# Kernel tuning notes

Measured on AMD Instinct MI355X. Metric: run time of the kernel, lower is better.

## Reference

```python
import jax, jax.numpy as jnp
import numpy as np

B, L, D = 32, 1024, 1024
NEG = -1.0e9


def setup_inputs() -> dict:
    key = jax.random.key(0)
    ks = jax.random.split(key, 12)
    s = 1.0 / np.sqrt(D)
    # random prefix lengths in [L//2, L] -> prefix-ones attention mask
    lengths = jax.random.randint(ks[0], (B,), L // 2, L + 1)
    attention_mask = (jnp.arange(L)[None, :] < lengths[:, None]).astype(jnp.int32)
    return {
        "output": jax.random.normal(ks[1], (B, L, D), jnp.float32),
        "context": jax.random.normal(ks[2], (B, L, D), jnp.float32),
        "attention_mask": attention_mask,
        "Wo": jax.random.uniform(ks[3], (D, D), jnp.float32, -s, s),   # output_trans
        "bo": jnp.zeros((D,), jnp.float32),
        "Wc": jax.random.uniform(ks[4], (D, D), jnp.float32, -s, s),   # context_trans
        "bc": jnp.zeros((D,), jnp.float32),
        "Wb": jax.random.uniform(ks[5], (D, D), jnp.float32, -s, s),   # bilinear (no bias)
        "Wu": jax.random.uniform(ks[6], (1, D), jnp.float32, -s, s),   # U
        "bu": jnp.zeros((1,), jnp.float32),
        "Wv": jax.random.uniform(ks[7], (1, D), jnp.float32, -s, s),   # V
        "bv": jnp.zeros((1,), jnp.float32),
        "Wf": jax.random.uniform(ks[8], (D, 2 * D), jnp.float32, -s, s),  # fc: 2D -> D
        "bf": jnp.zeros((D,), jnp.float32),
    }


def reference(output, context, attention_mask, Wo, bo, Wc, bc, Wb, Wu, bu, Wv, bv, Wf, bf):
    mask_f = attention_mask.astype(output.dtype)          # [B,L]
    lengths = jnp.sum(mask_f, axis=-1)                    # [B]
    key_padding = jnp.where(attention_mask > 0, 0.0, NEG).astype(output.dtype)  # [B,L]

    o_t = output @ Wo.T + bo                              # [B,L,D] output_trans
    c_t = context @ Wc.T + bc                             # [B,L,D] context_trans
    # biaffine: bilinear(o_t) @ c_t^T + U(output) + V(context)^T
    attn = jnp.einsum("bqd,bkd->bqk", o_t @ Wb.T, c_t)    # [B,L,L]
    attn = attn + (output @ Wu.T + bu)                    # [B,L,1] broadcast over keys
    attn = attn + jnp.swapaxes(context @ Wv.T + bv, 1, 2) # [B,1,L] broadcast over queries
    attn = attn + key_padding[:, None, :]
    attn = jax.nn.softmax(attn, axis=-1)

    mix = jnp.einsum("bqk,bkd->bqd", attn, context)       # [B,L,D]
    combined = jnp.concatenate([output, mix], axis=-1)    # [B,L,2D]
    out = jnp.tanh(combined @ Wf.T + bf)                  # [B,L,D]
    # masked mean pooling over sequence
    pooled = jnp.sum(out * mask_f[:, :, None], axis=1) / lengths[:, None]  # [B,D]
    return pooled
```

## Files before the change

### kernel.cpp

```cpp
#include <hip/hip_runtime.h>
#include <hip/hip_fp16.h>
#include <cstdint>
#include <initializer_list>

#define BATCH 32
#define LSEQ 1024
#define DDIM 1024

typedef unsigned short u16;
typedef unsigned int u32;
typedef __bf16 bf16x8 __attribute__((ext_vector_type(8)));
typedef float f32x4 __attribute__((ext_vector_type(4)));

__device__ __forceinline__ u16 f2bf(float f) {
  u32 u = __float_as_uint(f);
  u32 r = (u + 0x7FFFu + ((u >> 16) & 1u)) >> 16;
  return (u16)r;
}
__device__ __forceinline__ float bf2f(u16 h) {
  return __uint_as_float(((u32)h) << 16);
}
__device__ __forceinline__ float tanh_fast(float x) {
  float xx = fminf(fmaxf(x, -15.f), 15.f);
  float t = __expf(2.f * xx);
  return (t - 1.f) / (t + 1.f);
}

__device__ __forceinline__ void gload_lds16(const void* g, void* l) {
  __builtin_amdgcn_global_load_lds(
      (__attribute__((address_space(1))) void*)(uintptr_t)g,
      (__attribute__((address_space(3))) void*)(u32)(uintptr_t)l,
      16, 0, 0);
}

__global__ __launch_bounds__(256) void len_kernel(const int* __restrict__ amask,
                                                  int* __restrict__ lenb) {
  int b = blockIdx.x;
  int4 m = ((const int4*)(amask + (size_t)b * LSEQ))[threadIdx.x];
  int s = m.x + m.y + m.z + m.w;
#pragma unroll
  for (int o = 32; o; o >>= 1) s += __shfl_xor(s, o);
  __shared__ int r[4];
  if ((threadIdx.x & 63) == 0) r[threadIdx.x >> 6] = s;
  __syncthreads();
  if (threadIdx.x == 0) lenb[b] = (r[0] + r[1]) + (r[2] + r[3]);
}

__global__ __launch_bounds__(256) void cvt_kernel(const float* __restrict__ in,
                                                  u16* __restrict__ out, int n4) {
  int i = blockIdx.x * 256 + threadIdx.x;
  if (i >= n4) return;
  float4 f = ((const float4*)in)[i];
  ushort4 o;
  o.x = f2bf(f.x); o.y = f2bf(f.y); o.z = f2bf(f.z); o.w = f2bf(f.w);
  ((ushort4*)out)[i] = o;
}

__global__ __launch_bounds__(256) void transpose_cv(const float* __restrict__ in,
                                                    u16* __restrict__ outT,
                                                    u16* __restrict__ outN,
                                                    const float* __restrict__ wv2,
                                                    float* __restrict__ vpart,
                                                    int vn) {
  __shared__ u16 tile[64][65];
  size_t boff = (size_t)blockIdx.z * (LSEQ * DDIM);
  int k0 = blockIdx.x * 64;
  int d0 = blockIdx.y * 64;
  int tx = threadIdx.x & 63;
  int ty = threadIdx.x >> 6;
  float wv = vpart ? wv2[d0 + tx] : 0.f;
#pragma unroll
  for (int r = ty; r < 64; r += 4) {
    float f = in[boff + (size_t)(k0 + r) * DDIM + d0 + tx];
    u16 h = f2bf(f);
    tile[r][tx] = h;
    if (outN) outN[boff + (size_t)(k0 + r) * DDIM + d0 + tx] = h;
    if (vpart) {
      float p = f * wv;
#pragma unroll
      for (int o = 32; o; o >>= 1) p += __shfl_xor(p, o);
      if (tx == 0) vpart[(size_t)blockIdx.y * vn + blockIdx.z * LSEQ + k0 + r] = p;
    }
  }
  __syncthreads();
#pragma unroll
  for (int r = ty; r < 64; r += 4)
    outT[boff + (size_t)(d0 + r) * LSEQ + k0 + tx] = tile[tx][r];
}

__global__ __launch_bounds__(256) void vred_kernel(const float* __restrict__ vpart,
                                                   float* __restrict__ vbuf, int vn) {
  int i = blockIdx.x * 256 + threadIdx.x;
  if (i >= vn) return;
  float s = 0.f;
#pragma unroll
  for (int p = 0; p < 16; ++p) s += vpart[(size_t)p * vn + i];
  vbuf[i] = s;
}

__global__ __launch_bounds__(256) void rowdot_kernel(const float* __restrict__ x,
                                                     const float* __restrict__ w,
                                                     float* __restrict__ out) {
  int row = blockIdx.x;
  const float* p = x + (size_t)row * DDIM;
  int tid = threadIdx.x;
  float4 a = ((const float4*)p)[tid];
  float4 ww = ((const float4*)w)[tid];
  float s = a.x * ww.x + a.y * ww.y + a.z * ww.z + a.w * ww.w;
#pragma unroll
  for (int o = 32; o; o >>= 1) s += __shfl_xor(s, o);
  __shared__ float r[4];
  if ((tid & 63) == 0) r[tid >> 6] = s;
  __syncthreads();
  if (tid == 0) out[row] = (r[0] + r[1]) + (r[2] + r[3]);
}

__global__ __launch_bounds__(256) void w2_kernel(const float* __restrict__ Wv,
                                                 const float* __restrict__ bbo,
                                                 const float* __restrict__ Wc,
                                                 float* __restrict__ wv2) {
  int d = blockIdx.x * 256 + threadIdx.x;
  float s = Wv[d];
  for (int e = 0; e < DDIM; ++e) s += bbo[e] * Wc[(size_t)e * DDIM + d];
  wv2[d] = s;
}

template <int OUT_F32, int HAS_BIAS, int DO_TANH, int ZBATCH>
__global__ __launch_bounds__(256) void gemm_nt(
    const u16* __restrict__ A1, const u16* __restrict__ A2, int ksplit,
    const u16* __restrict__ Bw, const float* __restrict__ bias,
    void* __restrict__ Cout, int K, int lda, int ldb, int ldc,
    long long sA, long long sB, long long sC, int nm, int nn, int nz) {
  __shared__ u16 As[4096];
  __shared__ u16 Bs[4096];

  const int id = blockIdx.x;
  int bz, mb, nb;
  if (ZBATCH) {
    if ((nz & 7) == 0) {
      int x = id & 7; int j = id >> 3; int pb = nm * nn;
      bz = x + 8 * (j / pb);
      int in_ = j % pb; nb = in_ % nn; mb = in_ / nn;
    } else { bz = id % nz; int t = id / nz; nb = t % nn; mb = t / nn; }
  } else {
    bz = 0;
    if ((nm & 7) == 0) {
      int mg = id & 7; int t = id >> 3; int nmg = nm >> 3;
      nb = t % nn; mb = mg * nmg + t / nn;
    } else { nb = id % nn; mb = id / nn; }
  }

  const int tid = threadIdx.x;
  const int lane = tid & 63;
  const int wid = tid >> 6;
  const int wm = wid >> 1;
  const int wn = wid & 1;
  const int m0 = mb * 128;
  const int n0 = nb * 128;

  const u16* a1 = A1 + (size_t)bz * sA;
  const u16* a2 = A2 + (size_t)bz * sA;
  const u16* bw = Bw + (size_t)bz * sB;

  const int srow = wid * 16 + (lane >> 2);
  const int skof = (lane & 3) * 8;

  f32x4 acc[4][4] = {};

  for (int k0 = 0; k0 < K; k0 += 32) {
    const u16* ab; int kk;
    if (k0 < ksplit) { ab = a1; kk = k0; } else { ab = a2; kk = k0 - ksplit; }
    const u16* asrc = ab + (size_t)(m0 + srow) * lda + kk + skof;
    const u16* bsrc = bw + (size_t)(n0 + srow) * ldb + k0 + skof;
    gload_lds16(asrc, &As[wid * 512]);
    gload_lds16(asrc + (size_t)64 * lda, &As[2048 + wid * 512]);
    gload_lds16(bsrc, &Bs[wid * 512]);
    gload_lds16(bsrc + (size_t)64 * ldb, &Bs[2048 + wid * 512]);
    __syncthreads();

    bf16x8 af[4], bfv[4];
#pragma unroll
    for (int i = 0; i < 4; ++i) {
      af[i] = *(const bf16x8*)&As[(wm * 64 + i * 16 + (lane & 15)) * 32 + (lane >> 4) * 8];
      bfv[i] = *(const bf16x8*)&Bs[(wn * 64 + i * 16 + (lane & 15)) * 32 + (lane >> 4) * 8];
    }
#pragma unroll
    for (int i = 0; i < 4; ++i)
#pragma unroll
      for (int j = 0; j < 4; ++j)
        acc[i][j] = __builtin_amdgcn_mfma_f32_16x16x32_bf16(af[i], bfv[j], acc[i][j], 0, 0, 0);
    __syncthreads();
  }

  const int crow = (lane >> 4) * 4;
  const int ccol = lane & 15;
#pragma unroll
  for (int i = 0; i < 4; ++i) {
#pragma unroll
    for (int j = 0; j < 4; ++j) {
      int r0 = m0 + wm * 64 + i * 16 + crow;
      int c = n0 + wn * 64 + j * 16 + ccol;
      float bb = HAS_BIAS ? bias[c] : 0.f;
#pragma unroll
      for (int t = 0; t < 4; ++t) {
        float v = acc[i][j][t] + bb;
        if (DO_TANH) v = tanh_fast(v);
        size_t idx = (size_t)bz * sC + (size_t)(r0 + t) * ldc + c;
        if (OUT_F32) ((float*)Cout)[idx] = v;
        else ((u16*)Cout)[idx] = f2bf(v);
      }
    }
  }
}

template <int OUTT, int HAS_BIAS, int DO_TANH, int ZBATCH, int MASK, int POOL>
__global__ __launch_bounds__(512, 1) void gemm8p(
    const u16* __restrict__ A1, const u16* __restrict__ A2, int ksplit,
    const u16* __restrict__ Bw, const float* __restrict__ bias, long long sBias,
    void* __restrict__ Cout, int K, int lda, int ldb, int ldc,
    long long sA, long long sB, long long sC, int nm, int nn, int nz,
    const int* __restrict__ lenb, float* __restrict__ pf) {
  __shared__ __align__(16) u16 A0[16384];
  __shared__ __align__(16) u16 A1s[16384];
  __shared__ __align__(16) u16 B0[16384];
  __shared__ __align__(16) u16 B1s[16384];

  const int id = blockIdx.x;
  int bz, mb, nb;
  if (ZBATCH) {
    if ((nz & 7) == 0) {
      int x = id & 7; int j = id >> 3; int pb = nm * nn;
      bz = x + 8 * (j / pb);
      int in_ = j % pb; nb = in_ % nn; mb = in_ / nn;
    } else { bz = id % nz; int t = id / nz; nb = t % nn; mb = t / nn; }
  } else {
    bz = 0;
    if ((nm & 7) == 0) {
      int mg = id & 7; int t = id >> 3; int nmg = nm >> 3;
      nb = t % nn; mb = mg * nmg + t / nn;
    } else { nb = id % nn; mb = id / nn; }
  }

  const int m0 = mb * 256;
  const int n0 = nb * 256;

  int Keff = K;
  if (MASK) {
    if (MASK & 1) {
      int lb = ZBATCH ? bz : (m0 >> 10);
      int lm = ZBATCH ? m0 : (m0 & 1023);
      if (lm >= lenb[lb]) return;
    }
    if (MASK & 2) {
      if (n0 >= lenb[bz]) return;
    }
    if (MASK & 4) {
      Keff = (lenb[bz] + 63) & ~63;
    }
  }
  const int NT = Keff >> 6;

  const int tid = threadIdx.x;
  const int lane = tid & 63;
  const int wid = tid >> 6;
  const int wm = wid >> 2;
  const int wn = wid & 3;

  const u16* a1 = A1 + (size_t)bz * sA;
  const u16* a2 = A2 + (size_t)bz * sA;
  const u16* bw = Bw + (size_t)bz * sB;

  const int stR = lane >> 3;
  const int stS = ((lane & 7) ^ (lane >> 3)) * 8;
  const int a1w = (wid < 4) ? wid : 4 + wid;
  const int a2w = (wid < 4) ? 4 + wid : 8 + wid;

  const int frr = lane & 15;
  const int fo0 = frr * 64 + (((lane >> 4)) ^ (frr & 7)) * 8;
  const int fo1 = frr * 64 + ((4 + (lane >> 4)) ^ (frr & 7)) * 8;

  f32x4 acc[8][4] = {};

#define STG_A(tt, buf, st)                                                   \
  do {                                                                       \
    int kb = (tt) << 6; const u16* g; int gk;                                \
    if (kb < ksplit) { g = a1; gk = kb; } else { g = a2; gk = kb - ksplit; } \
    const u16* src = g + (size_t)(m0 + (st) * 16 + stR) * lda + gk + stS;    \
    gload_lds16(src, (buf) + (st) * 1024);                                   \
    gload_lds16(src + (size_t)8 * lda, (buf) + (st) * 1024 + 512);           \
  } while (0)
#define STG_B(tt, buf, st)                                                   \
  do {                                                                       \
    int kb = (tt) << 6;                                                      \
    const u16* src = bw + (size_t)(n0 + (st) * 16 + stR) * ldb + kb + stS;   \
    gload_lds16(src, (buf) + (st) * 1024);                                   \
    gload_lds16(src + (size_t)8 * ldb, (buf) + (st) * 1024 + 512);           \
  } while (0)
#define BARR                                                                 \
  do {                                                                       \
    __builtin_amdgcn_s_barrier();                                            \
    asm volatile("s_waitcnt lgkmcnt(0)" ::: "memory");                       \
    __builtin_amdgcn_sched_barrier(0);                                       \
  } while (0)
#define MM(mb_)                                                              \
  do {                                                                       \
    __builtin_amdgcn_s_setprio(1);                                           \
    _Pragma("unroll") for (int mh = 0; mh < 2; ++mh)                         \
    _Pragma("unroll") for (int n = 0; n < 4; ++n) {                          \
      acc[(mb_) + mh][n] = __builtin_amdgcn_mfma_f32_16x16x32_bf16(          \
          afr[mh][0], bfr[n][0], acc[(mb_) + mh][n], 0, 0, 0);               \
      acc[(mb_) + mh][n] = __builtin_amdgcn_mfma_f32_16x16x32_bf16(          \
          afr[mh][1], bfr[n][1], acc[(mb_) + mh][n], 0, 0, 0);               \
    }                                                                        \
    __builtin_amdgcn_s_setprio(0);                                           \
  } while (0)
#define LDA2(Ab, mb_)                                                        \
  do {                                                                       \
    afr[0][0] = *(const bf16x8*)((Ab) + (wm * 8 + (mb_)) * 1024 + fo0);      \
    afr[0][1] = *(const bf16x8*)((Ab) + (wm * 8 + (mb_)) * 1024 + fo1);      \
    afr[1][0] = *(const bf16x8*)((Ab) + (wm * 8 + (mb_) + 1) * 1024 + fo0);  \
    afr[1][1] = *(const bf16x8*)((Ab) + (wm * 8 + (mb_) + 1) * 1024 + fo1);  \
  } while (0)

#define TILE(t, Ab, Bb, An, Bn)                                              \
  do {                                                                       \
    const bool stg = (t) + 1 < NT;                                           \
    bf16x8 bfr[4][2], afr[2][2];                                             \
    _Pragma("unroll") for (int n = 0; n < 4; ++n) {                          \
      bfr[n][0] = *(const bf16x8*)((Bb) + (wn * 4 + n) * 1024 + fo0);        \
      bfr[n][1] = *(const bf16x8*)((Bb) + (wn * 4 + n) * 1024 + fo1);        \
    }                                                                        \
    LDA2(Ab, 0);                                                             \
    if (stg) STG_B((t) + 1, Bn, wid);                                        \
    BARR; MM(0);                                                             \
    LDA2(Ab, 2);                                                             \
    if (stg) {                                                               \
      STG_B((t) + 1, Bn, 8 + wid);                                           \
      asm volatile("s_waitcnt vmcnt(4)" ::: "memory");                       \
    } else {                                                                 \
      asm volatile("s_waitcnt vmcnt(0)" ::: "memory");                       \
    }                                                                        \
    BARR; MM(2);                                                             \
    LDA2(Ab, 4);                                                             \
    if (stg) STG_A((t) + 1, An, a1w);                                        \
    BARR; MM(4);                                                             \
    LDA2(Ab, 6);                                                             \
    if (stg) {                                                               \
      STG_A((t) + 1, An, a2w);                                               \
      asm volatile("s_waitcnt vmcnt(2)" ::: "memory");                       \
    }                                                                        \
    BARR; MM(6);                                                             \
  } while (0)

  STG_A(0, A0, wid); STG_A(0, A0, wid + 8);
  STG_B(0, B0, wid); STG_B(0, B0, wid + 8);
  asm volatile("s_waitcnt vmcnt(0)" ::: "memory");
  __builtin_amdgcn_s_barrier();

  for (int t = 0; t < NT; t += 2) {
    TILE(t, A0, B0, A1s, B1s);
    if (t + 1 < NT) TILE(t + 1, A1s, B1s, A0, B0);
  }
#undef TILE
#undef LDA2
#undef MM
#undef BARR
#undef STG_A
#undef STG_B

  const int crow = (lane >> 4) * 4;
  const int ccol = lane & 15;

  if (POOL) {
    const int b = m0 >> 10;
    const int lenv = lenb[b];
    const int qbase = (m0 & 1023) + wm * 128 + crow;
    float csum[4] = {0.f, 0.f, 0.f, 0.f};
#pragma unroll
    for (int j = 0; j < 4; ++j) {
      int c = n0 + wn * 64 + j * 16 + ccol;
      float bb = bias[c];
#pragma unroll
      for (int i = 0; i < 8; ++i) {
#pragma unroll
        for (int t = 0; t < 4; ++t) {
          int q = qbase + i * 16 + t;
          float v = tanh_fast(acc[i][j][t] + bb);
          csum[j] += (q < lenv) ? v : 0.f;
        }
      }
    }
    float* red = (float*)A0;
#pragma unroll
    for (int j = 0; j < 4; ++j) {
      float cs = csum[j];
      cs += __shfl_xor(cs, 16);
      cs += __shfl_xor(cs, 32);
      if (lane < 16) red[(wm * 4 + wn) * 64 + j * 16 + lane] = cs;
    }
    __syncthreads();
    if (tid < 256) {
      int wnn = tid >> 6, cl = tid & 63;
      float v = red[(0 * 4 + wnn) * 64 + cl] + red[(1 * 4 + wnn) * 64 + cl];
      pf[(size_t)mb * 1024 + n0 + wnn * 64 + cl] = v;
    }
    return;
  }

#pragma unroll
  for (int i = 0; i < 8; ++i) {
#pragma unroll
    for (int j = 0; j < 4; ++j) {
      int r0 = m0 + wm * 128 + i * 16 + crow;
      int c = n0 + wn * 64 + j * 16 + ccol;
      float bb = HAS_BIAS ? bias[(size_t)bz * sBias + c] : 0.f;
#pragma unroll
      for (int t = 0; t < 4; ++t) {
        float v = acc[i][j][t] + bb;
        if (DO_TANH) v = tanh_fast(v);
        size_t idx = (size_t)bz * sC + (size_t)(r0 + t) * ldc + c;
        if (OUTT == 0) {
          ((float*)Cout)[idx] = v;
        } else if (OUTT == 1) {
          ((u16*)Cout)[idx] = f2bf(v);
        } else {
          __half hv = __float2half(v);
          ((u16*)Cout)[idx] = __half_as_ushort(hv);
        }
      }
    }
  }
}

__global__ __launch_bounds__(256) void softmax_rows(const u16* __restrict__ logits,
                                                    const int* __restrict__ amask,
                                                    u16* __restrict__ P,
                                                    const int* __restrict__ lenb) {
  const int row = blockIdx.x;
  const int b = row >> 10;
  const int q = row & 1023;
  if (q >= lenb[b]) return;
  const u16* lg = logits + (size_t)row * LSEQ;
  u16* prow = P + (size_t)row * LSEQ;
  const int tid = threadIdx.x;

  ushort4 lraw = ((const ushort4*)lg)[tid];
  int4 mk4 = ((const int4*)(amask + (b << 10)))[tid];

  float x[4];
  int mk[4] = {mk4.x, mk4.y, mk4.z, mk4.w};
  x[0] = __half2float(__ushort_as_half(lraw.x));
  x[1] = __half2float(__ushort_as_half(lraw.y));
  x[2] = __half2float(__ushort_as_half(lraw.z));
  x[3] = __half2float(__ushort_as_half(lraw.w));

  float vmax = -3.0e38f;
#pragma unroll
  for (int i = 0; i < 4; ++i) {
    if (!mk[i]) x[i] = -3.0e38f;
    vmax = fmaxf(vmax, x[i]);
  }
#pragma unroll
  for (int o = 32; o; o >>= 1) vmax = fmaxf(vmax, __shfl_xor(vmax, o));
  __shared__ float sred[4];
  if ((tid & 63) == 0) sred[tid >> 6] = vmax;
  __syncthreads();
  vmax = fmaxf(fmaxf(sred[0], sred[1]), fmaxf(sred[2], sred[3]));
  float s = 0.f, e[4];
#pragma unroll
  for (int i = 0; i < 4; ++i) {
    e[i] = mk[i] ? __expf(x[i] - vmax) : 0.f;
    s += e[i];
  }
#pragma unroll
  for (int o = 32; o; o >>= 1) s += __shfl_xor(s, o);
  __shared__ float ssum[4];
  if ((tid & 63) == 0) ssum[tid >> 6] = s;
  __syncthreads();
  s = (ssum[0] + ssum[1]) + (ssum[2] + ssum[3]);
  float inv = 1.f / s;
  ushort4 o4;
  o4.x = f2bf(e[0] * inv);
  o4.y = f2bf(e[1] * inv);
  o4.z = f2bf(e[2] * inv);
  o4.w = f2bf(e[3] * inv);
  ((ushort4*)prow)[tid] = o4;
}

__global__ __launch_bounds__(256) void pool_final(const float* __restrict__ pf,
                                                  const int* __restrict__ lenb,
                                                  float* __restrict__ out) {
  int idx = blockIdx.x * 256 + threadIdx.x;
  int b = idx >> 10;
  int d = idx & 1023;
  int len = lenb[b];
  float s = 0.f;
#pragma unroll
  for (int qc = 0; qc < 4; ++qc)
    if (qc * 256 < len) s += pf[(size_t)(b * 4 + qc) * 1024 + d];
  out[idx] = s / (float)len;
}

extern "C" void kernel_launch(void* const* d_in, const int* in_sizes, int n_in,
                              void* d_out, int out_size, void* d_ws, size_t ws_size,
                              hipStream_t stream) {
  const float* output = (const float*)d_in[0];
  const float* context = (const float*)d_in[1];
  const int* amask = (const int*)d_in[2];
  const float* Wo = (const float*)d_in[3];
  const float* bo = (const float*)d_in[4];
  const float* Wc = (const float*)d_in[5];
  const float* Wb = (const float*)d_in[7];
  const float* Wv = (const float*)d_in[10];
  const float* Wf = (const float*)d_in[12];
  const float* bfb = (const float*)d_in[13];
  float* out = (float*)d_out;
  (void)n_in; (void)in_sizes; (void)out_size;

  const size_t LD2 = (size_t)LSEQ * DDIM * 2;
  const size_t fixed_b = (size_t)24 * (1 << 20);
  const size_t per_b = 4 * LD2 + (size_t)LSEQ * LSEQ * 2 + 80 * LSEQ + 4096;
  int G = 1;
  for (int g : {32, 16, 8, 4, 2, 1}) {
    if (fixed_b + (size_t)g * per_b <= ws_size) { G = g; break; }
  }
  const int NG = BATCH / G;
  const int VN = G * LSEQ;

  char* ws = (char*)d_ws;
  size_t off = 0;
  auto alloc = [&](size_t bytes) {
    char* p = ws + off;
    off += (bytes + 255) & ~(size_t)255;
    return p;
  };
  const size_t W2 = (size_t)DDIM * DDIM * 2;
  u16* wb_bf = (u16*)alloc(W2);
  u16* wf_bf = (u16*)alloc(2 * W2);
  u16* woT_bf = (u16*)alloc(W2);
  u16* wcT_bf = (u16*)alloc(W2);
  u16* wboT_bf = (u16*)alloc(W2);
  u16* mt_bf = (u16*)alloc(W2);
  float* bbo = (float*)alloc(DDIM * 4);
  float* wv2 = (float*)alloc(DDIM * 4);
  int* lenb = (int*)alloc(BATCH * 4);
  float* pf = (float*)alloc((size_t)BATCH * 4 * DDIM * 4);
  u16* out_g = (u16*)alloc((size_t)G * LD2);
  u16* ctx_g = (u16*)alloc((size_t)G * LD2);
  u16* ctxT_g = (u16*)alloc((size_t)G * LD2);
  u16* y_g = (u16*)alloc((size_t)G * LD2);
  u16* logits = (u16*)alloc((size_t)G * LSEQ * LSEQ * 2);
  float* vbuf = (float*)alloc((size_t)VN * 4);
  float* vpart = (float*)alloc((size_t)16 * VN * 4);

  dim3 blk(256), blk8(512);
  const long long M1 = (long long)LSEQ * DDIM;
  const int BIG = 1 << 30;

  len_kernel<<<dim3(BATCH), blk, 0, stream>>>(amask, lenb);
  cvt_kernel<<<dim3(1024), blk, 0, stream>>>(Wb, wb_bf, DDIM * DDIM / 4);
  cvt_kernel<<<dim3(2048), blk, 0, stream>>>(Wf, wf_bf, DDIM * 2 * DDIM / 4);
  transpose_cv<<<dim3(16, 16, 1), blk, 0, stream>>>(Wo, woT_bf, nullptr, nullptr, nullptr, 0);
  transpose_cv<<<dim3(16, 16, 1), blk, 0, stream>>>(Wc, wcT_bf, nullptr, nullptr, nullptr, 0);
  rowdot_kernel<<<dim3(1024), blk, 0, stream>>>(Wb, bo, bbo);
  w2_kernel<<<dim3(4), blk, 0, stream>>>(Wv, bbo, Wc, wv2);
  gemm_nt<0, 0, 0, 0><<<dim3(64), blk, 0, stream>>>(
      woT_bf, woT_bf, BIG, wb_bf, nullptr, wboT_bf,
      1024, 1024, 1024, 1024, 0, 0, 0, 8, 8, 1);
  gemm_nt<0, 0, 0, 0><<<dim3(64), blk, 0, stream>>>(
      wcT_bf, wcT_bf, BIG, wboT_bf, nullptr, mt_bf,
      1024, 1024, 1024, 1024, 0, 0, 0, 8, 8, 1);

  for (int grp = 0; grp < NG; ++grp) {
    const int gb = grp * G;
    const float* outp = output + (size_t)gb * LSEQ * DDIM;
    const float* ctxp = context + (size_t)gb * LSEQ * DDIM;
    const int* amp = amask + (size_t)gb * LSEQ;
    const int* lnp = lenb + gb;
    const int n4 = G * LSEQ * DDIM / 4;

    cvt_kernel<<<dim3(n4 / 256), blk, 0, stream>>>(outp, out_g, n4);
    transpose_cv<<<dim3(16, 16, G), blk, 0, stream>>>(ctxp, ctxT_g, ctx_g, wv2, vpart, VN);
    vred_kernel<<<dim3(VN / 256), blk, 0, stream>>>(vpart, vbuf, VN);

    gemm8p<1, 0, 0, 0, 1, 0><<<dim3(G * 16), blk8, 0, stream>>>(
        out_g, out_g, BIG, mt_bf, nullptr, 0, y_g,
        1024, 1024, 1024, 1024, 0, 0, 0, G * 4, 4, 1, lnp, nullptr);
    gemm8p<2, 1, 0, 1, 3, 0><<<dim3(G * 16), blk8, 0, stream>>>(
        y_g, y_g, BIG, ctx_g, vbuf, 1024, logits,
        1024, 1024, 1024, 1024, M1, M1, M1, 4, 4, G, lnp, nullptr);
    softmax_rows<<<dim3(G * LSEQ), blk, 0, stream>>>(logits, amp, y_g, lnp);
    gemm8p<1, 0, 0, 1, 5, 0><<<dim3(G * 16), blk8, 0, stream>>>(
        y_g, y_g, BIG, ctxT_g, nullptr, 0, ctx_g,
        1024, 1024, 1024, 1024, M1, M1, M1, 4, 4, G, lnp, nullptr);
    gemm8p<1, 1, 1, 0, 1, 1><<<dim3(G * 16), blk8, 0, stream>>>(
        out_g, ctx_g, 1024, wf_bf, bfb, 0, nullptr,
        2048, 1024, 2048, 1024, 0, 0, 0, G * 4, 4, 1, lnp,
        pf + (size_t)gb * 4 * DDIM);
  }
  pool_final<<<dim3(128), blk, 0, stream>>>(pf, lenb, out);
}
```

Baseline: 578.6 us.

## Replace 512-thread 256x256 GEMM with 256-thread 256x128 two-blocks-per-CU kernel

The main bf16 MFMA GEMM goes from 8 waves on a 256x256 tile with K=64 stages and a staged four-phase barrier pipeline to 4 waves on a 256x128 tile with K=32 stages. The new kernel allows two blocks per CU and issues all next-tile loads up front, with one barrier per tile. The goal is to hide latency through inter-block occupancy rather than intra-block software pipelining, and to get finer tile granularity for the masked early-exit tiles. In exchange, data reuse per block is lower, the B matrix is reloaded more often, and there is one barrier per 32-wide K step.

```diff
diff --git a/kernel.cpp b/kernel.cpp
--- a/kernel.cpp
+++ b/kernel.cpp
@@ -214,16 +214,16 @@
 }
 
 template <int OUTT, int HAS_BIAS, int DO_TANH, int ZBATCH, int MASK, int POOL>
-__global__ __launch_bounds__(512, 1) void gemm8p(
+__global__ __launch_bounds__(256, 2) void gemm2b(
     const u16* __restrict__ A1, const u16* __restrict__ A2, int ksplit,
     const u16* __restrict__ Bw, const float* __restrict__ bias, long long sBias,
     void* __restrict__ Cout, int K, int lda, int ldb, int ldc,
     long long sA, long long sB, long long sC, int nm, int nn, int nz,
     const int* __restrict__ lenb, float* __restrict__ pf) {
-  __shared__ __align__(16) u16 A0[16384];
-  __shared__ __align__(16) u16 A1s[16384];
-  __shared__ __align__(16) u16 B0[16384];
-  __shared__ __align__(16) u16 B1s[16384];
+  __shared__ __align__(16) u16 A0[8192];
+  __shared__ __align__(16) u16 A1s[8192];
+  __shared__ __align__(16) u16 B0[4096];
+  __shared__ __align__(16) u16 B1s[4096];
 
   const int id = blockIdx.x;
   int bz, mb, nb;
@@ -242,7 +242,7 @@
   }
 
   const int m0 = mb * 256;
-  const int n0 = nb * 256;
+  const int n0 = nb * 128;
 
   int Keff = K;
   if (MASK) {
@@ -255,105 +255,86 @@
       if (n0 >= lenb[bz]) return;
     }
     if (MASK & 4) {
-      Keff = (lenb[bz] + 63) & ~63;
-    }
-  }
-  const int NT = Keff >> 6;
+      Keff = (lenb[bz] + 31) & ~31;
+    }
+  }
+  const int NT = Keff >> 5;
 
   const int tid = threadIdx.x;
   const int lane = tid & 63;
   const int wid = tid >> 6;
-  const int wm = wid >> 2;
-  const int wn = wid & 3;
-
+  const int wm = wid >> 1;
+  const int wn = wid & 1;
   const u16* a1 = A1 + (size_t)bz * sA;
   const u16* a2 = A2 + (size_t)bz * sA;
   const u16* bw = Bw + (size_t)bz * sB;
 
-  const int stR = lane >> 3;
-  const int stS = ((lane & 7) ^ (lane >> 3)) * 8;
-  const int a1w = (wid < 4) ? wid : 4 + wid;
-  const int a2w = (wid < 4) ? 4 + wid : 8 + wid;
+  const int stR = lane >> 2;
+  const int stS = (((lane & 3) ^ ((lane >> 2) & 3))) * 8;
 
   const int frr = lane & 15;
-  const int fo0 = frr * 64 + (((lane >> 4)) ^ (frr & 7)) * 8;
-  const int fo1 = frr * 64 + ((4 + (lane >> 4)) ^ (frr & 7)) * 8;
+  const int fo = frr * 32 + ((((lane >> 4) & 3) ^ (frr & 3)) * 8);
 
   f32x4 acc[8][4] = {};
 
 #define STG_A(tt, buf, st)                                                   \
   do {                                                                       \
-    int kb = (tt) << 6; const u16* g; int gk;                                \
+    int kb = (tt) << 5; const u16* g; int gk;                                \
     if (kb < ksplit) { g = a1; gk = kb; } else { g = a2; gk = kb - ksplit; } \
-    const u16* src = g + (size_t)(m0 + (st) * 16 + stR) * lda + gk + stS;    \
-    gload_lds16(src, (buf) + (st) * 1024);                                   \
-    gload_lds16(src + (size_t)8 * lda, (buf) + (st) * 1024 + 512);           \
+    gload_lds16(g + (size_t)(m0 + (st) * 16 + stR) * lda + gk + stS,         \
+                (buf) + (st) * 512);                                         \
   } while (0)
 #define STG_B(tt, buf, st)                                                   \
   do {                                                                       \
-    int kb = (tt) << 6;                                                      \
-    const u16* src = bw + (size_t)(n0 + (st) * 16 + stR) * ldb + kb + stS;   \
-    gload_lds16(src, (buf) + (st) * 1024);                                   \
-    gload_lds16(src + (size_t)8 * ldb, (buf) + (st) * 1024 + 512);           \
+    int kb = (tt) << 5;                                                      \
+    gload_lds16(bw + (size_t)(n0 + (st) * 16 + stR) * ldb + kb + stS,        \
+                (buf) + (st) * 512);                                         \
   } while (0)
-#define BARR                                                                 \
+#define WAITL(n)                                                             \
   do {                                                                       \
-    __builtin_amdgcn_s_barrier();                                            \
-    asm volatile("s_waitcnt lgkmcnt(0)" ::: "memory");                       \
+    asm volatile("s_waitcnt lgkmcnt(" #n ")" ::: "memory");                  \
     __builtin_amdgcn_sched_barrier(0);                                       \
   } while (0)
-#define MM(mb_)                                                              \
+#define MM4(base, ar)                                                        \
   do {                                                                       \
     __builtin_amdgcn_s_setprio(1);                                           \
-    _Pragma("unroll") for (int mh = 0; mh < 2; ++mh)                         \
-    _Pragma("unroll") for (int n = 0; n < 4; ++n) {                          \
-      acc[(mb_) + mh][n] = __builtin_amdgcn_mfma_f32_16x16x32_bf16(          \
-          afr[mh][0], bfr[n][0], acc[(mb_) + mh][n], 0, 0, 0);               \
-      acc[(mb_) + mh][n] = __builtin_amdgcn_mfma_f32_16x16x32_bf16(          \
-          afr[mh][1], bfr[n][1], acc[(mb_) + mh][n], 0, 0, 0);               \
-    }                                                                        \
+    _Pragma("unroll") for (int i = 0; i < 4; ++i)                            \
+    _Pragma("unroll") for (int n = 0; n < 4; ++n)                            \
+      acc[(base) + i][n] = __builtin_amdgcn_mfma_f32_16x16x32_bf16(          \
+          ar[i], bfr[n], acc[(base) + i][n], 0, 0, 0);                       \
     __builtin_amdgcn_s_setprio(0);                                           \
-  } while (0)
-#define LDA2(Ab, mb_)                                                        \
-  do {                                                                       \
-    afr[0][0] = *(const bf16x8*)((Ab) + (wm * 8 + (mb_)) * 1024 + fo0);      \
-    afr[0][1] = *(const bf16x8*)((Ab) + (wm * 8 + (mb_)) * 1024 + fo1);      \
-    afr[1][0] = *(const bf16x8*)((Ab) + (wm * 8 + (mb_) + 1) * 1024 + fo0);  \
-    afr[1][1] = *(const bf16x8*)((Ab) + (wm * 8 + (mb_) + 1) * 1024 + fo1);  \
   } while (0)
 
 #define TILE(t, Ab, Bb, An, Bn)                                              \
   do {                                                                       \
     const bool stg = (t) + 1 < NT;                                           \
-    bf16x8 bfr[4][2], afr[2][2];                                             \
-    _Pragma("unroll") for (int n = 0; n < 4; ++n) {                          \
-      bfr[n][0] = *(const bf16x8*)((Bb) + (wn * 4 + n) * 1024 + fo0);        \
-      bfr[n][1] = *(const bf16x8*)((Bb) + (wn * 4 + n) * 1024 + fo1);        \
+    if (stg) {                                                               \
+      STG_A((t) + 1, An, wid);                                               \
+      STG_A((t) + 1, An, wid + 4);                                           \
+      STG_A((t) + 1, An, wid + 8);                                           \
+      STG_A((t) + 1, An, wid + 12);                                          \
+      STG_B((t) + 1, Bn, wid);                                               \
+      STG_B((t) + 1, Bn, wid + 4);                                           \
     }                                                                        \
-    LDA2(Ab, 0);                                                             \
-    if (stg) STG_B((t) + 1, Bn, wid);                                        \
-    BARR; MM(0);                                                             \
-    LDA2(Ab, 2);                                                             \
-    if (stg) {                                                               \
-      STG_B((t) + 1, Bn, 8 + wid);                                           \
-      asm volatile("s_waitcnt vmcnt(4)" ::: "memory");                       \
-    } else {                                                                 \
-      asm volatile("s_waitcnt vmcnt(0)" ::: "memory");                       \
-    }                                                                        \
-    BARR; MM(2);                                                             \
-    LDA2(Ab, 4);                                                             \
-    if (stg) STG_A((t) + 1, An, a1w);                                        \
-    BARR; MM(4);                                                             \
-    LDA2(Ab, 6);                                                             \
-    if (stg) {                                                               \
-      STG_A((t) + 1, An, a2w);                                               \
-      asm volatile("s_waitcnt vmcnt(2)" ::: "memory");                       \
-    }                                                                        \
-    BARR; MM(6);                                                             \
+    bf16x8 bfr[4], aA[4], aB[4];                                             \
+    _Pragma("unroll") for (int n = 0; n < 4; ++n)                            \
+      bfr[n] = *(const bf16x8*)((Bb) + (wn * 4 + n) * 512 + fo);             \
+    _Pragma("unroll") for (int i = 0; i < 4; ++i)                            \
+      aA[i] = *(const bf16x8*)((Ab) + (wm * 8 + i) * 512 + fo);              \
+    _Pragma("unroll") for (int i = 0; i < 4; ++i)                            \
+      aB[i] = *(const bf16x8*)((Ab) + (wm * 8 + 4 + i) * 512 + fo);          \
+    WAITL(4);                                                                \
+    MM4(0, aA);                                                              \
+    WAITL(0);                                                                \
+    MM4(4, aB);                                                              \
+    asm volatile("s_waitcnt vmcnt(0)" ::: "memory");                         \
+    __builtin_amdgcn_s_barrier();                                            \
+    __builtin_amdgcn_sched_barrier(0);                                       \
   } while (0)
 
-  STG_A(0, A0, wid); STG_A(0, A0, wid + 8);
-  STG_B(0, B0, wid); STG_B(0, B0, wid + 8);
+  STG_A(0, A0, wid); STG_A(0, A0, wid + 4);
+  STG_A(0, A0, wid + 8); STG_A(0, A0, wid + 12);
+  STG_B(0, B0, wid); STG_B(0, B0, wid + 4);
   asm volatile("s_waitcnt vmcnt(0)" ::: "memory");
   __builtin_amdgcn_s_barrier();
 
@@ -362,9 +343,8 @@
     if (t + 1 < NT) TILE(t + 1, A1s, B1s, A0, B0);
   }
 #undef TILE
-#undef LDA2
-#undef MM
-#undef BARR
+#undef MM4
+#undef WAITL
 #undef STG_A
 #undef STG_B
 
@@ -396,12 +376,12 @@
       float cs = csum[j];
       cs += __shfl_xor(cs, 16);
       cs += __shfl_xor(cs, 32);
-      if (lane < 16) red[(wm * 4 + wn) * 64 + j * 16 + lane] = cs;
+      if (lane < 16) red[(wm * 2 + wn) * 64 + j * 16 + lane] = cs;
     }
     __syncthreads();
-    if (tid < 256) {
+    if (tid < 128) {
       int wnn = tid >> 6, cl = tid & 63;
-      float v = red[(0 * 4 + wnn) * 64 + cl] + red[(1 * 4 + wnn) * 64 + cl];
+      float v = red[(0 * 2 + wnn) * 64 + cl] + red[(1 * 2 + wnn) * 64 + cl];
       pf[(size_t)mb * 1024 + n0 + wnn * 64 + cl] = v;
     }
     return;
@@ -553,7 +533,7 @@
   float* vbuf = (float*)alloc((size_t)VN * 4);
   float* vpart = (float*)alloc((size_t)16 * VN * 4);
 
-  dim3 blk(256), blk8(512);
+  dim3 blk(256);
   const long long M1 = (long long)LSEQ * DDIM;
   const int BIG = 1 << 30;
 
@@ -583,19 +563,19 @@
     transpose_cv<<<dim3(16, 16, G), blk, 0, stream>>>(ctxp, ctxT_g, ctx_g, wv2, vpart, VN);
     vred_kernel<<<dim3(VN / 256), blk, 0, stream>>>(vpart, vbuf, VN);
 
-    gemm8p<1, 0, 0, 0, 1, 0><<<dim3(G * 16), blk8, 0, stream>>>(
+    gemm2b<1, 0, 0, 0, 1, 0><<<dim3(G * 32), blk, 0, stream>>>(
         out_g, out_g, BIG, mt_bf, nullptr, 0, y_g,
-        1024, 1024, 1024, 1024, 0, 0, 0, G * 4, 4, 1, lnp, nullptr);
-    gemm8p<2, 1, 0, 1, 3, 0><<<dim3(G * 16), blk8, 0, stream>>>(
+        1024, 1024, 1024, 1024, 0, 0, 0, G * 4, 8, 1, lnp, nullptr);
+    gemm2b<2, 1, 0, 1, 3, 0><<<dim3(G * 32), blk, 0, stream>>>(
         y_g, y_g, BIG, ctx_g, vbuf, 1024, logits,
-        1024, 1024, 1024, 1024, M1, M1, M1, 4, 4, G, lnp, nullptr);
+        1024, 1024, 1024, 1024, M1, M1, M1, 4, 8, G, lnp, nullptr);
     softmax_rows<<<dim3(G * LSEQ), blk, 0, stream>>>(logits, amp, y_g, lnp);
-    gemm8p<1, 0, 0, 1, 5, 0><<<dim3(G * 16), blk8, 0, stream>>>(
+    gemm2b<1, 0, 0, 1, 5, 0><<<dim3(G * 32), blk, 0, stream>>>(
         y_g, y_g, BIG, ctxT_g, nullptr, 0, ctx_g,
-        1024, 1024, 1024, 1024, M1, M1, M1, 4, 4, G, lnp, nullptr);
-    gemm8p<1, 1, 1, 0, 1, 1><<<dim3(G * 16), blk8, 0, stream>>>(
+        1024, 1024, 1024, 1024, M1, M1, M1, 4, 8, G, lnp, nullptr);
+    gemm2b<1, 1, 1, 0, 1, 1><<<dim3(G * 32), blk, 0, stream>>>(
         out_g, ctx_g, 1024, wf_bf, bfb, 0, nullptr,
-        2048, 1024, 2048, 1024, 0, 0, 0, G * 4, 4, 1, lnp,
+        2048, 1024, 2048, 1024, 0, 0, 0, G * 4, 8, 1, lnp,
         pf + (size_t)gb * 4 * DDIM);
   }
   pool_final<<<dim3(128), blk, 0, stream>>>(pf, lenb, out);
```

New measurement: 610.6 us. 1.06x slower.
